# Kernel optimization log

Measured on AMD Instinct MI355X. Metric: run time of the kernel, lower is better.

## Reference

```python
import jax, jax.numpy as jnp
import numpy as np

D_L = 64
HIDDEN = 64
CUBE = (D_L + 1) ** 3  # 274625


def setup_inputs() -> dict:
    key = jax.random.key(0)
    ks = jax.random.split(key, 9)
    B = 512
    l = jax.random.normal(ks[0], (B, D_L), dtype=jnp.float32)
    a = jax.random.normal(ks[1], (B, D_L), dtype=jnp.float32)
    v = jax.random.normal(ks[2], (B, D_L), dtype=jnp.float32)
    # Linear params (xavier-ish scale)
    W1 = jax.random.normal(ks[3], (CUBE, HIDDEN), dtype=jnp.float32) * (1.0 / np.sqrt(CUBE))
    b1 = jnp.zeros((HIDDEN,), dtype=jnp.float32)
    W2 = jax.random.normal(ks[4], (HIDDEN, HIDDEN), dtype=jnp.float32) * (1.0 / np.sqrt(HIDDEN))
    b2 = jnp.zeros((HIDDEN,), dtype=jnp.float32)
    W3 = jax.random.normal(ks[5], (HIDDEN, D_L), dtype=jnp.float32) * (1.0 / np.sqrt(HIDDEN))
    b3 = jnp.zeros((D_L,), dtype=jnp.float32)
    return {"l": l, "a": a, "v": v, "W1": W1, "b1": b1, "W2": W2, "b2": b2, "W3": W3, "b3": b3}


def reference(l, a, v, W1, b1, W2, b2, W3, b3):
    B = a.shape[0]
    ones = jnp.ones((B, 1), dtype=a.dtype)
    a_h = jnp.concatenate([ones, a], axis=1)  # [B, d+1]
    v_h = jnp.concatenate([ones, v], axis=1)
    t_h = jnp.concatenate([ones, l], axis=1)
    # fusion[b, i, j, k] = a_h[b,i] * v_h[b,j] * t_h[b,k]; flattened row-major (i,j,k)
    fusion = jnp.einsum('bi,bj,bk->bijk', a_h, v_h, t_h).reshape(B, -1)  # [B, (d+1)^3]
    h = jnp.tanh(fusion @ W1 + b1)
    h = jnp.tanh(h @ W2 + b2)
    out = jnp.tanh(h @ W3 + b3)
    return out
```

## Files before the change

kernel.cpp:

```cpp
#include <hip/hip_runtime.h>
#include <hip/hip_fp16.h>


typedef _Float16 f16;
typedef f16 f16x8 __attribute__((ext_vector_type(8)));
typedef f16 f16x2 __attribute__((ext_vector_type(2)));
typedef float f32x4 __attribute__((ext_vector_type(4)));

#define WS_AT      0
#define WS_VT      131072
#define WS_A16     262144
#define WS_V16     327680
#define WS_L16     393216
#define WS_PART    458752

__global__ __launch_bounds__(256) void prep_kernel(
    const float* __restrict__ l, const float* __restrict__ a, const float* __restrict__ v,
    float* __restrict__ aT, float* __restrict__ vT,
    f16* __restrict__ a16, f16* __restrict__ v16, f16* __restrict__ l16)
{
  int g = blockIdx.x * 256 + threadIdx.x;
  int which = g >> 15;
  int idx = g & 32767;
  switch (which) {
    case 0: aT[idx] = a[((idx & 511) << 6) + (idx >> 9)]; break;
    case 1: vT[idx] = v[((idx & 511) << 6) + (idx >> 9)]; break;
    case 2: a16[idx] = (f16)a[idx]; break;
    case 3: v16[idx] = (f16)v[idx]; break;
    case 4: l16[idx] = (f16)l[idx]; break;
  }
}

__device__ __forceinline__ void seg_decode(int s, int& ia, int& iv, int& isel,
                                           int& rowbase, int& rowstride) {
  if (s < 4096)      { int i = s >> 6, j = s & 63; ia = i; iv = j; isel = 0;
                       rowbase = (i+1)*4225 + (j+1)*65 + 1; rowstride = 1; }
  else if (s < 4160) { int i = s - 4096; ia = i; iv = -1; isel = 2;
                       rowbase = (i+1)*4225 + 65; rowstride = 65; }
  else if (s < 4224) { int i = s - 4160; ia = i; iv = -1; isel = 0;
                       rowbase = (i+1)*4225 + 1; rowstride = 1; }
  else if (s < 4288) { int j = s - 4224; ia = -1; iv = j; isel = 0;
                       rowbase = (j+1)*65 + 1; rowstride = 1; }
  else if (s == 4288){ ia = -1; iv = -1; isel = 1; rowbase = 4225; rowstride = 4225; }
  else if (s == 4289){ ia = -1; iv = -1; isel = 2; rowbase = 65;   rowstride = 65; }
  else if (s == 4290){ ia = -1; iv = -1; isel = 0; rowbase = 1;    rowstride = 1; }
  else               { ia = -2; iv = -1; isel = 0; rowbase = 1;    rowstride = 1; }
}

__global__ __launch_bounds__(1024, 4) void fusion_gemm(
    const float* __restrict__ W1,
    const float* __restrict__ aT, const float* __restrict__ vT,
    const f16* __restrict__ a16, const f16* __restrict__ v16, const f16* __restrict__ l16,
    f16* __restrict__ partials)
{
  __shared__ f16 btile[4][64 * 64];
  __shared__ f16 pl[4][512];

  const int tid  = threadIdx.x;
  const int bid  = blockIdx.x;
  const int lane = tid & 63;
  const int wave = tid >> 6;
  const int l15  = lane & 15;
  const int l4   = lane >> 4;
  const int h    = tid >> 9;
  const int t9   = tid & 511;
  const int n_st = t9 & 63;
  const int g_st = t9 >> 6;

  f16x8 lfrag[2][2];
  #pragma unroll
  for (int mt = 0; mt < 2; ++mt) {
    int row = (wave << 5) + (mt << 4) + l15;
    #pragma unroll
    for (int ks = 0; ks < 2; ++ks)
      lfrag[mt][ks] = *(const f16x8*)(l16 + (row << 6) + (ks << 5) + (l4 << 3));
  }

  f32x4 acc[2][4] = {};

  float wv[2][8];
  float sp[2][2];

#define ISSUE_LOADS(SET, SEG) do {                                              \
    int ia_, iv_, isel_, rb_, rs_; seg_decode((SEG), ia_, iv_, isel_, rb_, rs_);\
    const int rs64_ = rs_ << 6;                                                 \
    const float* src_ = W1 + (size_t)rb_ * 64 + (size_t)(g_st << 3) * rs64_ + n_st; \
    _Pragma("unroll")                                                           \
    for (int r_ = 0; r_ < 8; ++r_) wv[SET][r_] = src_[(size_t)r_ * rs64_];      \
    sp[SET][0] = (ia_ >= 0) ? aT[(ia_ << 9) + t9] : (ia_ == -1 ? 1.0f : 0.0f);  \
    sp[SET][1] = (iv_ >= 0) ? vT[(iv_ << 9) + t9] : 1.0f;                       \
  } while (0)

  ISSUE_LOADS(0, bid * 18 + h);

  #pragma unroll
  for (int pp = 0; pp < 9; ++pp) {
    const int cur = pp & 1;
    const int sbw = (cur << 1) + h;
    {
      f16x8 c;
      if (cur == 0) {
        #pragma unroll
        for (int r = 0; r < 8; ++r) c[r] = (f16)wv[0][r];
      } else {
        #pragma unroll
        for (int r = 0; r < 8; ++r) c[r] = (f16)wv[1][r];
      }
      *(f16x8*)&btile[sbw][(n_st << 6) + ((g_st ^ (n_st & 7)) << 3)] = c;
      pl[sbw][t9] = (f16)(sp[cur][0] * sp[cur][1]);
    }
    if (pp < 8) {
      if (cur == 0) ISSUE_LOADS(1, bid * 18 + (pp + 1) * 2 + h);
      else          ISSUE_LOADS(0, bid * 18 + (pp + 1) * 2 + h);
    }
    asm volatile("s_waitcnt lgkmcnt(0)\n\ts_barrier" ::: "memory");
    __builtin_amdgcn_sched_barrier(0);

    #pragma unroll
    for (int sidx = 0; sidx < 2; ++sidx) {
      const int sb = (cur << 1) + sidx;
      int s = bid * 18 + pp * 2 + sidx;
      int ia_, iv_, isel, rb_, rs_;
      seg_decode(s, ia_, iv_, isel, rb_, rs_);
      const f16* gsrc = (isel == 1) ? a16 : v16;
      #pragma unroll
      for (int ks = 0; ks < 2; ++ks) {
        f16x8 bf[4];
        #pragma unroll
        for (int nt = 0; nt < 4; ++nt) {
          int n = (nt << 4) + l15;
          bf[nt] = *(const f16x8*)&btile[sb][(n << 6) + ((((ks << 2) + l4) ^ (n & 7)) << 3)];
        }
        #pragma unroll
        for (int mt = 0; mt < 2; ++mt) {
          int row = (wave << 5) + (mt << 4) + l15;
          f16 ps = pl[sb][row];
          f16x8 lv;
          if (isel == 0) lv = lfrag[mt][ks];
          else           lv = *(const f16x8*)(gsrc + (row << 6) + (ks << 5) + (l4 << 3));
          f16x2 ps2 = { ps, ps };
          f16x8 av;
          f16x2* lvp = (f16x2*)&lv;
          f16x2* avp = (f16x2*)&av;
          avp[0] = lvp[0] * ps2; avp[1] = lvp[1] * ps2;
          avp[2] = lvp[2] * ps2; avp[3] = lvp[3] * ps2;
          #pragma unroll
          for (int nt = 0; nt < 4; ++nt)
            acc[mt][nt] = __builtin_amdgcn_mfma_f32_16x16x32_f16(av, bf[nt], acc[mt][nt], 0, 0, 0);
        }
      }
    }
  }
#undef ISSUE_LOADS

  #pragma unroll
  for (int mt = 0; mt < 2; ++mt)
    #pragma unroll
    for (int nt = 0; nt < 4; ++nt)
      #pragma unroll
      for (int r = 0; r < 4; ++r) {
        int row = (wave << 5) + (mt << 4) + (l4 << 2) + r;
        int col = (nt << 4) + l15;
        partials[((size_t)row << 14) + (bid << 6) + col] = (f16)acc[mt][nt][r];
      }
}

__global__ __launch_bounds__(256) void tail_kernel(
    const f16* __restrict__ partials, const float* __restrict__ W1, const float* __restrict__ b1,
    const float* __restrict__ W2, const float* __restrict__ b2,
    const float* __restrict__ W3, const float* __restrict__ b3, float* __restrict__ out)
{
  __shared__ float red[256][8];
  __shared__ float hbuf[64];
  __shared__ float h2buf[64];
  const int row = blockIdx.x;
  const int t = threadIdx.x;
  const f16* base = partials + ((size_t)row << 14);

  float s[8] = {0.f,0.f,0.f,0.f,0.f,0.f,0.f,0.f};
  #pragma unroll
  for (int j = 0; j < 8; ++j) {
    f16x8 v = *(const f16x8*)(base + (((j << 8) + t) << 3));
    #pragma unroll
    for (int e = 0; e < 8; ++e) s[e] += (float)v[e];
  }
  #pragma unroll
  for (int e = 0; e < 8; ++e) red[t][e] = s[e];
  __syncthreads();
  if (t < 64) {
    float acc = b1[t] + W1[t];
    #pragma unroll
    for (int k = 0; k < 32; ++k) acc += red[(t >> 3) + (k << 3)][t & 7];
    hbuf[t] = tanhf(acc);
  }
  __syncthreads();
  if (t < 64) {
    float acc = b2[t];
    #pragma unroll 8
    for (int k = 0; k < 64; ++k) acc += hbuf[k] * W2[(k << 6) + t];
    h2buf[t] = tanhf(acc);
  }
  __syncthreads();
  if (t < 64) {
    float acc = b3[t];
    #pragma unroll 8
    for (int k = 0; k < 64; ++k) acc += h2buf[k] * W3[(k << 6) + t];
    out[(row << 6) + t] = tanhf(acc);
  }
}

extern "C" void kernel_launch(void* const* d_in, const int* in_sizes, int n_in,
                              void* d_out, int out_size, void* d_ws, size_t ws_size,
                              hipStream_t stream) {
  const float* l  = (const float*)d_in[0];
  const float* a  = (const float*)d_in[1];
  const float* v  = (const float*)d_in[2];
  const float* W1 = (const float*)d_in[3];
  const float* b1 = (const float*)d_in[4];
  const float* W2 = (const float*)d_in[5];
  const float* b2 = (const float*)d_in[6];
  const float* W3 = (const float*)d_in[7];
  const float* b3 = (const float*)d_in[8];
  float* out = (float*)d_out;

  char* ws = (char*)d_ws;
  float* aT  = (float*)(ws + WS_AT);
  float* vT  = (float*)(ws + WS_VT);
  f16*   a16 = (f16*)(ws + WS_A16);
  f16*   v16 = (f16*)(ws + WS_V16);
  f16*   l16 = (f16*)(ws + WS_L16);
  f16*   partials = (f16*)(ws + WS_PART);

  hipLaunchKernelGGL(prep_kernel, dim3(640), dim3(256), 0, stream,
                     l, a, v, aT, vT, a16, v16, l16);
  hipLaunchKernelGGL(fusion_gemm, dim3(256), dim3(1024), 0, stream,
                     W1, aT, vT, a16, v16, l16, partials);
  hipLaunchKernelGGL(tail_kernel, dim3(512), dim3(256), 0, stream,
                     partials, W1, b1, W2, b2, W3, b3, out);
}
```

Measured before the change: 63.04 us.

## Fold input prep into fused GEMM and restructure to 512-thread blocks

```diff
diff --git a/kernel.cpp b/kernel.cpp
--- a/kernel.cpp
+++ b/kernel.cpp
@@ -5,31 +5,7 @@
 typedef _Float16 f16;
 typedef f16 f16x8 __attribute__((ext_vector_type(8)));
 typedef f16 f16x2 __attribute__((ext_vector_type(2)));
-typedef float f32x4 __attribute__((ext_vector_type(4)));
-
-#define WS_AT      0
-#define WS_VT      131072
-#define WS_A16     262144
-#define WS_V16     327680
-#define WS_L16     393216
-#define WS_PART    458752
-
-__global__ __launch_bounds__(256) void prep_kernel(
-    const float* __restrict__ l, const float* __restrict__ a, const float* __restrict__ v,
-    float* __restrict__ aT, float* __restrict__ vT,
-    f16* __restrict__ a16, f16* __restrict__ v16, f16* __restrict__ l16)
-{
-  int g = blockIdx.x * 256 + threadIdx.x;
-  int which = g >> 15;
-  int idx = g & 32767;
-  switch (which) {
-    case 0: aT[idx] = a[((idx & 511) << 6) + (idx >> 9)]; break;
-    case 1: vT[idx] = v[((idx & 511) << 6) + (idx >> 9)]; break;
-    case 2: a16[idx] = (f16)a[idx]; break;
-    case 3: v16[idx] = (f16)v[idx]; break;
-    case 4: l16[idx] = (f16)l[idx]; break;
-  }
-}
+typedef float fx4 __attribute__((ext_vector_type(4)));
 
 __device__ __forceinline__ void seg_decode(int s, int& ia, int& iv, int& isel,
                                            int& rowbase, int& rowstride) {
@@ -47,14 +23,25 @@
   else               { ia = -2; iv = -1; isel = 0; rowbase = 1;    rowstride = 1; }
 }
 
-__global__ __launch_bounds__(1024, 4) void fusion_gemm(
-    const float* __restrict__ W1,
-    const float* __restrict__ aT, const float* __restrict__ vT,
-    const f16* __restrict__ a16, const f16* __restrict__ v16, const f16* __restrict__ l16,
+__device__ __forceinline__ f16x8 cvt8(fx4 x0, fx4 x1) {
+  f16x8 f;
+  f[0]=(f16)x0[0]; f[1]=(f16)x0[1]; f[2]=(f16)x0[2]; f[3]=(f16)x0[3];
+  f[4]=(f16)x1[0]; f[5]=(f16)x1[1]; f[6]=(f16)x1[2]; f[7]=(f16)x1[3];
+  return f;
+}
+__device__ __forceinline__ f16x8 cvt8s(float a0,float a1,float a2,float a3,
+                                       float a4,float a5,float a6,float a7){
+  f16x8 f; f[0]=(f16)a0; f[1]=(f16)a1; f[2]=(f16)a2; f[3]=(f16)a3;
+  f[4]=(f16)a4; f[5]=(f16)a5; f[6]=(f16)a6; f[7]=(f16)a7; return f;
+}
+
+__global__ __launch_bounds__(512, 2) void fusion_gemm(
+    const float* __restrict__ W1, const float* __restrict__ a,
+    const float* __restrict__ v, const float* __restrict__ l,
     f16* __restrict__ partials)
 {
-  __shared__ f16 btile[4][64 * 64];
-  __shared__ f16 pl[4][512];
+  __shared__ f16 btile[2][4096];
+  __shared__ f16 pl[2][512];
 
   const int tid  = threadIdx.x;
   const int bid  = blockIdx.x;
@@ -62,104 +49,105 @@
   const int wave = tid >> 6;
   const int l15  = lane & 15;
   const int l4   = lane >> 4;
-  const int h    = tid >> 9;
-  const int t9   = tid & 511;
-  const int n_st = t9 & 63;
-  const int g_st = t9 >> 6;
-
-  f16x8 lfrag[2][2];
-  #pragma unroll
-  for (int mt = 0; mt < 2; ++mt) {
-    int row = (wave << 5) + (mt << 4) + l15;
-    #pragma unroll
-    for (int ks = 0; ks < 2; ++ks)
-      lfrag[mt][ks] = *(const f16x8*)(l16 + (row << 6) + (ks << 5) + (l4 << 3));
-  }
-
-  f32x4 acc[2][4] = {};
-
-  float wv[2][8];
-  float sp[2][2];
-
-#define ISSUE_LOADS(SET, SEG) do {                                              \
-    int ia_, iv_, isel_, rb_, rs_; seg_decode((SEG), ia_, iv_, isel_, rb_, rs_);\
-    const int rs64_ = rs_ << 6;                                                 \
-    const float* src_ = W1 + (size_t)rb_ * 64 + (size_t)(g_st << 3) * rs64_ + n_st; \
-    _Pragma("unroll")                                                           \
-    for (int r_ = 0; r_ < 8; ++r_) wv[SET][r_] = src_[(size_t)r_ * rs64_];      \
-    sp[SET][0] = (ia_ >= 0) ? aT[(ia_ << 9) + t9] : (ia_ == -1 ? 1.0f : 0.0f);  \
-    sp[SET][1] = (iv_ >= 0) ? vT[(iv_ << 9) + t9] : 1.0f;                       \
+  const int n_st = tid & 63;
+  const int kg   = wave;
+
+  f16x8 lfrag[4][2];
+  #pragma unroll
+  for (int mt = 0; mt < 4; ++mt) {
+    int row = (wave << 6) + (mt << 4) + l15;
+    #pragma unroll
+    for (int ks = 0; ks < 2; ++ks) {
+      const float* p = l + (row << 6) + (ks << 5) + (l4 << 3);
+      lfrag[mt][ks] = cvt8(*(const fx4*)p, *(const fx4*)(p + 4));
+    }
+  }
+
+  fx4 acc[4][4] = {};
+
+  float wv[3][8];
+  float spa[3], spv[3];
+  const int segbase = bid * 17;
+
+#define ISSUE(SL, SEG) do {                                                     \
+    int s_ = (SEG); int ia_, iv_, isel_, rb_, rs_;                              \
+    seg_decode(s_, ia_, iv_, isel_, rb_, rs_);                                  \
+    const int rstep_ = rs_ << 6;                                                \
+    const float* src_ = W1 + (size_t)(rb_ + (kg << 3) * rs_) * 64 + n_st;       \
+    wv[SL][0] = src_[0];                  wv[SL][1] = src_[rstep_];             \
+    wv[SL][2] = src_[rstep_ * 2];         wv[SL][3] = src_[rstep_ * 3];         \
+    wv[SL][4] = src_[(size_t)rstep_ * 4]; wv[SL][5] = src_[(size_t)rstep_ * 5]; \
+    wv[SL][6] = src_[(size_t)rstep_ * 6]; wv[SL][7] = src_[(size_t)rstep_ * 7]; \
+    spa[SL] = (ia_ >= 0) ? a[(tid << 6) + ia_] : (ia_ == -1 ? 1.0f : 0.0f);     \
+    spv[SL] = (iv_ >= 0) ? v[(tid << 6) + iv_] : 1.0f;                          \
   } while (0)
 
-  ISSUE_LOADS(0, bid * 18 + h);
-
-  #pragma unroll
-  for (int pp = 0; pp < 9; ++pp) {
-    const int cur = pp & 1;
-    const int sbw = (cur << 1) + h;
-    {
-      f16x8 c;
-      if (cur == 0) {
-        #pragma unroll
-        for (int r = 0; r < 8; ++r) c[r] = (f16)wv[0][r];
-      } else {
-        #pragma unroll
-        for (int r = 0; r < 8; ++r) c[r] = (f16)wv[1][r];
-      }
-      *(f16x8*)&btile[sbw][(n_st << 6) + ((g_st ^ (n_st & 7)) << 3)] = c;
-      pl[sbw][t9] = (f16)(sp[cur][0] * sp[cur][1]);
-    }
-    if (pp < 8) {
-      if (cur == 0) ISSUE_LOADS(1, bid * 18 + (pp + 1) * 2 + h);
-      else          ISSUE_LOADS(0, bid * 18 + (pp + 1) * 2 + h);
-    }
-    asm volatile("s_waitcnt lgkmcnt(0)\n\ts_barrier" ::: "memory");
-    __builtin_amdgcn_sched_barrier(0);
-
-    #pragma unroll
-    for (int sidx = 0; sidx < 2; ++sidx) {
-      const int sb = (cur << 1) + sidx;
-      int s = bid * 18 + pp * 2 + sidx;
-      int ia_, iv_, isel, rb_, rs_;
-      seg_decode(s, ia_, iv_, isel, rb_, rs_);
-      const f16* gsrc = (isel == 1) ? a16 : v16;
-      #pragma unroll
-      for (int ks = 0; ks < 2; ++ks) {
-        f16x8 bf[4];
-        #pragma unroll
-        for (int nt = 0; nt < 4; ++nt) {
-          int n = (nt << 4) + l15;
-          bf[nt] = *(const f16x8*)&btile[sb][(n << 6) + ((((ks << 2) + l4) ^ (n & 7)) << 3)];
-        }
-        #pragma unroll
-        for (int mt = 0; mt < 2; ++mt) {
-          int row = (wave << 5) + (mt << 4) + l15;
-          f16 ps = pl[sb][row];
-          f16x8 lv;
-          if (isel == 0) lv = lfrag[mt][ks];
-          else           lv = *(const f16x8*)(gsrc + (row << 6) + (ks << 5) + (l4 << 3));
-          f16x2 ps2 = { ps, ps };
-          f16x8 av;
-          f16x2* lvp = (f16x2*)&lv;
-          f16x2* avp = (f16x2*)&av;
-          avp[0] = lvp[0] * ps2; avp[1] = lvp[1] * ps2;
-          avp[2] = lvp[2] * ps2; avp[3] = lvp[3] * ps2;
-          #pragma unroll
-          for (int nt = 0; nt < 4; ++nt)
-            acc[mt][nt] = __builtin_amdgcn_mfma_f32_16x16x32_f16(av, bf[nt], acc[mt][nt], 0, 0, 0);
-        }
-      }
-    }
-  }
-#undef ISSUE_LOADS
-
-  #pragma unroll
-  for (int mt = 0; mt < 2; ++mt)
+#define BODY(IDX, SL, BUF) do {                                                 \
+         \
+    f16x8 c_ = cvt8s(wv[SL][0], wv[SL][1], wv[SL][2], wv[SL][3],                \
+                     wv[SL][4], wv[SL][5], wv[SL][6], wv[SL][7]);               \
+    *(f16x8*)&btile[BUF][(n_st << 6) + (((kg << 1) ^ ((n_st & 7) << 1)) << 2)] = c_; \
+    pl[BUF][tid] = (f16)(spa[SL] * spv[SL]);                                    \
+    if ((IDX) + 3 < 17) ISSUE(SL, segbase + (IDX) + 3);                         \
+    asm volatile("s_waitcnt lgkmcnt(0)\n\ts_barrier" ::: "memory");             \
+    __builtin_amdgcn_sched_barrier(0);                                          \
+    { int s_ = segbase + (IDX); int ia_, iv_, isel_, rb_, rs_;                  \
+      seg_decode(s_, ia_, iv_, isel_, rb_, rs_);                                \
+      const float* gsrc_ = (isel_ == 1) ? a : v;                                \
+      _Pragma("unroll")                                                         \
+      for (int ks = 0; ks < 2; ++ks) {                                          \
+        f16x8 bf_[4];                                                           \
+        _Pragma("unroll")                                                       \
+        for (int nt = 0; nt < 4; ++nt) {                                        \
+          int n_ = (nt << 4) + l15;                                             \
+          int c0_ = (ks << 3) + (l4 << 1);                                      \
+          bf_[nt] = *(const f16x8*)&btile[BUF][(n_ << 6) + ((c0_ ^ ((n_ & 7) << 1)) << 2)]; \
+        }                                                                       \
+        _Pragma("unroll")                                                       \
+        for (int mt = 0; mt < 4; ++mt) {                                        \
+          int row_ = (wave << 6) + (mt << 4) + l15;                             \
+          f16 ps_ = pl[BUF][row_];                                              \
+          f16x8 lv_;                                                            \
+          if (isel_ == 0) lv_ = lfrag[mt][ks];                                  \
+          else { const float* p_ = gsrc_ + (row_ << 6) + (ks << 5) + (l4 << 3); \
+                 lv_ = cvt8(*(const fx4*)p_, *(const fx4*)(p_ + 4)); }          \
+          f16x2 ps2_ = { ps_, ps_ };                                            \
+          f16x8 av_;                                                            \
+          ((f16x2*)&av_)[0] = ((f16x2*)&lv_)[0] * ps2_;                         \
+          ((f16x2*)&av_)[1] = ((f16x2*)&lv_)[1] * ps2_;                         \
+          ((f16x2*)&av_)[2] = ((f16x2*)&lv_)[2] * ps2_;                         \
+          ((f16x2*)&av_)[3] = ((f16x2*)&lv_)[3] * ps2_;                         \
+          _Pragma("unroll")                                                     \
+          for (int nt = 0; nt < 4; ++nt)                                        \
+            acc[mt][nt] = __builtin_amdgcn_mfma_f32_16x16x32_f16(av_, bf_[nt], acc[mt][nt], 0, 0, 0); \
+        }                                                                       \
+      }                                                                         \
+    }                                                                           \
+  } while (0)
+
+  ISSUE(0, segbase + 0);
+  ISSUE(1, segbase + 1);
+  ISSUE(2, segbase + 2);
+
+  #pragma unroll 1
+  for (int t = 0; t < 2; ++t) {
+    const int b6 = t * 6;
+    BODY(b6 + 0, 0, 0); BODY(b6 + 1, 1, 1); BODY(b6 + 2, 2, 0);
+    BODY(b6 + 3, 0, 1); BODY(b6 + 4, 1, 0); BODY(b6 + 5, 2, 1);
+  }
+  BODY(12, 0, 0); BODY(13, 1, 1); BODY(14, 2, 0);
+  BODY(15, 0, 1); BODY(16, 1, 0);
+
+#undef ISSUE
+#undef BODY
+
+  #pragma unroll
+  for (int mt = 0; mt < 4; ++mt)
     #pragma unroll
     for (int nt = 0; nt < 4; ++nt)
       #pragma unroll
       for (int r = 0; r < 4; ++r) {
-        int row = (wave << 5) + (mt << 4) + (l4 << 2) + r;
+        int row = (wave << 6) + (mt << 4) + (l4 << 2) + r;
         int col = (nt << 4) + l15;
         partials[((size_t)row << 14) + (bid << 6) + col] = (f16)acc[mt][nt][r];
       }
@@ -180,9 +168,9 @@
   float s[8] = {0.f,0.f,0.f,0.f,0.f,0.f,0.f,0.f};
   #pragma unroll
   for (int j = 0; j < 8; ++j) {
-    f16x8 v = *(const f16x8*)(base + (((j << 8) + t) << 3));
-    #pragma unroll
-    for (int e = 0; e < 8; ++e) s[e] += (float)v[e];
+    f16x8 vv = *(const f16x8*)(base + (((j << 8) + t) << 3));
+    #pragma unroll
+    for (int e = 0; e < 8; ++e) s[e] += (float)vv[e];
   }
   #pragma unroll
   for (int e = 0; e < 8; ++e) red[t][e] = s[e];
@@ -223,18 +211,10 @@
   const float* b3 = (const float*)d_in[8];
   float* out = (float*)d_out;
 
-  char* ws = (char*)d_ws;
-  float* aT  = (float*)(ws + WS_AT);
-  float* vT  = (float*)(ws + WS_VT);
-  f16*   a16 = (f16*)(ws + WS_A16);
-  f16*   v16 = (f16*)(ws + WS_V16);
-  f16*   l16 = (f16*)(ws + WS_L16);
-  f16*   partials = (f16*)(ws + WS_PART);
-
-  hipLaunchKernelGGL(prep_kernel, dim3(640), dim3(256), 0, stream,
-                     l, a, v, aT, vT, a16, v16, l16);
-  hipLaunchKernelGGL(fusion_gemm, dim3(256), dim3(1024), 0, stream,
-                     W1, aT, vT, a16, v16, l16, partials);
+  f16* partials = (f16*)d_ws;
+
+  hipLaunchKernelGGL(fusion_gemm, dim3(256), dim3(512), 0, stream,
+                     W1, a, v, l, partials);
   hipLaunchKernelGGL(tail_kernel, dim3(512), dim3(256), 0, stream,
                      partials, W1, b1, W2, b2, W3, b3, out);
 }
```

After: 91.70 us. 45.5% more time.
